# Optimization experiments

Hardware: AMD Instinct MI355X
Metric: run time of the kernel (lower is better)

Reference implementation:

```python
import jax, jax.numpy as jnp
import numpy as np

N_NODES = 50000
N_EDGES = 800000
N_GRAPHS = 2048
IN_DIM = 128
HID = 256
N_LAYERS = 4
BN_EPS = 1e-5


def setup_inputs() -> dict:
    key = jax.random.key(0)
    ks = jax.random.split(key, 12)
    x = jax.random.normal(ks[0], (N_NODES, IN_DIM), dtype=jnp.float32)
    edge_index = jax.random.randint(ks[1], (2, N_EDGES), 0, N_NODES, dtype=jnp.int64)
    batch = jnp.sort(jax.random.randint(ks[2], (N_NODES,), 0, N_GRAPHS, dtype=jnp.int64))
    convW0 = jax.random.normal(ks[3], (IN_DIM, HID), dtype=jnp.float32) * (IN_DIM ** -0.5)
    convWs = jax.random.normal(ks[4], (N_LAYERS - 1, HID, HID), dtype=jnp.float32) * (HID ** -0.5)
    convB = jnp.zeros((N_LAYERS, HID), dtype=jnp.float32)
    bn_gamma = jnp.ones((N_LAYERS, HID), dtype=jnp.float32)
    bn_beta = jnp.zeros((N_LAYERS, HID), dtype=jnp.float32)
    bn_mean = jnp.zeros((N_LAYERS, HID), dtype=jnp.float32)
    bn_var = jax.random.uniform(ks[5], (N_LAYERS, HID), dtype=jnp.float32, minval=0.5, maxval=1.5)
    lin1W = jax.random.normal(ks[6], (HID, HID // 2), dtype=jnp.float32) * (HID ** -0.5)
    lin1b = jnp.zeros((HID // 2,), dtype=jnp.float32)
    lin2W = jax.random.normal(ks[7], (HID // 2, 1), dtype=jnp.float32) * ((HID // 2) ** -0.5)
    lin2b = jnp.zeros((1,), dtype=jnp.float32)
    return dict(x=x, edge_index=edge_index, batch=batch, convW0=convW0, convWs=convWs,
                convB=convB, bn_gamma=bn_gamma, bn_beta=bn_beta, bn_mean=bn_mean,
                bn_var=bn_var, lin1W=lin1W, lin1b=lin1b, lin2W=lin2W, lin2b=lin2b)


def reference(x, edge_index, batch, convW0, convWs, convB, bn_gamma, bn_beta,
              bn_mean, bn_var, lin1W, lin1b, lin2W, lin2b):
    N = x.shape[0]
    src, dst = edge_index[0], edge_index[1]
    # degree with self-loops (PyG GCNConv default add_self_loops=True)
    deg = jnp.zeros((N,), dtype=x.dtype).at[dst].add(1.0) + 1.0
    dinv = deg ** -0.5
    enorm = (dinv[src] * dinv[dst])[:, None]      # [E,1]
    self_norm = (1.0 / deg)[:, None]              # [N,1] self-loop weight

    def gcn_conv(h, W, b):
        h = h @ W                                 # [N,H]
        agg = jax.ops.segment_sum(h[src] * enorm, dst, num_segments=N)
        return agg + h * self_norm + b

    Ws = [convW0] + [convWs[i] for i in range(convWs.shape[0])]
    for l in range(N_LAYERS):
        x = gcn_conv(x, Ws[l], convB[l])
        # eval-mode BatchNorm1d
        x = (x - bn_mean[l]) * jax.lax.rsqrt(bn_var[l] + BN_EPS) * bn_gamma[l] + bn_beta[l]
        x = jax.nn.relu(x)
        # dropout: identity in eval mode

    # global_mean_pool over graph ids
    sums = jax.ops.segment_sum(x, batch, num_segments=N_GRAPHS)      # [G,H]
    cnts = jax.ops.segment_sum(jnp.ones((N,), x.dtype), batch, num_segments=N_GRAPHS)
    pooled = sums / jnp.maximum(cnts, 1.0)[:, None]

    h = jax.nn.relu(pooled @ lin1W + lin1b)
    out = (h @ lin2W + lin2b).squeeze(-1)          # [G]
    return out
```

## Files before the change

kernel.cpp:

```cpp
#include <hip/hip_runtime.h>

#define N_NODES 50000
#define N_EDGES 800000
#define N_GRAPHS 2048
#define IN_DIM 128
#define HID 256
#define N_LAYERS 4
#define BN_EPS 1e-5f
#define NBIN 128
#define WSCALE 64.0f

#define EDGE_BLKS 3125
#define NODE_BLKS 196

typedef unsigned short ushort_t;
typedef float f32x4 __attribute__((ext_vector_type(4)));
typedef unsigned int u32x4 __attribute__((ext_vector_type(4)));
typedef _Float16 f16x8 __attribute__((ext_vector_type(8)));
typedef _Float16 f16x4 __attribute__((ext_vector_type(4)));

__device__ __forceinline__ void gl_lds16(const ushort_t* g, ushort_t* l) {
    __builtin_amdgcn_global_load_lds(
        (const __attribute__((address_space(1))) void*)g,
        (__attribute__((address_space(3))) void*)l, 16, 0, 0);
}

__global__ __launch_bounds__(256) void k_degbounds(const int* __restrict__ dst,
                                                   int* __restrict__ degi,
                                                   const int* __restrict__ batch,
                                                   int* __restrict__ gstart,
                                                   int* __restrict__ gend) {
    int bid = blockIdx.x;
    if (bid < EDGE_BLKS) {
        int e = bid * 256 + threadIdx.x;
        if (e < N_EDGES) atomicAdd(&degi[dst[e]], 1);
    } else {
        int n = (bid - EDGE_BLKS) * 256 + threadIdx.x;
        if (n >= N_NODES) return;
        int g = batch[n];
        if (n == 0 || batch[n - 1] != g) gstart[g] = n;
        if (n == N_NODES - 1 || batch[n + 1] != g) gend[g] = n + 1;
    }
}

__global__ __launch_bounds__(256) void k_nodeprep(const int* __restrict__ degi,
                                                  float* __restrict__ dinv,
                                                  float* __restrict__ selfn,
                                                  int* __restrict__ bins, int N) {
    __shared__ int lbin[NBIN];
    int t = threadIdx.x;
    if (t < NBIN) lbin[t] = 0;
    __syncthreads();
    int n = blockIdx.x * 256 + t;
    if (n < N) {
        int dg = degi[n];
        float d = 1.0f + (float)dg;
        dinv[n] = 1.0f / sqrtf(d);
        selfn[n] = 1.0f / d;
        atomicAdd(&lbin[min(dg, NBIN - 1)], 1);
    }
    __syncthreads();
    if (t < NBIN && lbin[t] > 0) atomicAdd(&bins[t], lbin[t]);
}

__global__ void k_binscan(const int* __restrict__ bins, int* __restrict__ binstart,
                          int* __restrict__ bincur, int* __restrict__ edgebase) {
    int t = threadIdx.x & 63;
    int d0 = 2 * t, d1 = 2 * t + 1;
    int a = bins[d0], b = bins[d1];
    int ea = a * d0, eb = b * d1;
    int s = a + b, es = ea + eb;
    int ps = s, pe = es;
    #pragma unroll
    for (int off = 1; off < 64; off <<= 1) {
        int u = __shfl_up(ps, off, 64);
        int v = __shfl_up(pe, off, 64);
        if (t >= off) { ps += u; pe += v; }
    }
    int exs = ps - s, exe = pe - es;
    binstart[d0] = exs;     bincur[d0] = exs;     edgebase[d0] = exe;
    binstart[d1] = exs + a; bincur[d1] = exs + a; edgebase[d1] = exe + ea;
}

__global__ __launch_bounds__(256) void k_assign(const int* __restrict__ degi,
                                                const int* __restrict__ binstart,
                                                const int* __restrict__ edgebase,
                                                const int* __restrict__ bins,
                                                int* __restrict__ bincur,
                                                int* __restrict__ perm, int* __restrict__ invperm,
                                                int2* __restrict__ meta, int* __restrict__ cursor,
                                                int N) {
    __shared__ int lbin[NBIN];
    __shared__ int lbase[NBIN];
    int t = threadIdx.x;
    if (t < NBIN) lbin[t] = 0;
    __syncthreads();
    int n = blockIdx.x * 256 + t;
    int d = 0, lrank = 0;
    if (n < N) {
        d = min(degi[n], NBIN - 1);
        lrank = atomicAdd(&lbin[d], 1);
    }
    __syncthreads();
    if (t < NBIN && lbin[t] > 0) lbase[t] = atomicAdd(&bincur[t], lbin[t]);
    __syncthreads();
    if (n < N) {
        int slot = lbase[d] + lrank;
        perm[slot] = n;
        invperm[n] = slot;
        int2 m;
        m.x = edgebase[d] + (slot - binstart[d]);
        m.y = bins[d] | (d << 20);
        meta[slot] = m;
        cursor[slot] = 0;
    }
}

__global__ __launch_bounds__(256) void k_fillprep(const int* __restrict__ src,
                                                  const int* __restrict__ dst,
                                                  const float* __restrict__ dinv,
                                                  const int* __restrict__ invperm,
                                                  const int2* __restrict__ meta,
                                                  int* __restrict__ cursor,
                                                  unsigned int* __restrict__ edata,
                                                  const float* __restrict__ gamma,
                                                  const float* __restrict__ beta,
                                                  const float* __restrict__ mean,
                                                  const float* __restrict__ var,
                                                  const float* __restrict__ bias,
                                                  const float* __restrict__ W0,
                                                  const float* __restrict__ Ws,
                                                  const float* __restrict__ x,
                                                  float* __restrict__ scale,
                                                  float* __restrict__ shift,
                                                  _Float16* __restrict__ Wh,
                                                  _Float16* __restrict__ Wl,
                                                  _Float16* __restrict__ X16) {
    int bid = blockIdx.x;
    if (bid < EDGE_BLKS) {
        int e = bid * 256 + threadIdx.x;
        if (e >= N_EDGES) return;
        int s = src[e], d = dst[e];
        int slot = invperm[d];
        int2 m = meta[slot];
        int j = atomicAdd(&cursor[slot], 1);
        int pos = m.x + j * (m.y & 0xFFFFF);
        _Float16 hw = (_Float16)(dinv[s] * dinv[d]);
        edata[pos] = ((unsigned int)__builtin_bit_cast(unsigned short, hw) << 16) |
                     (unsigned int)s;
        return;
    }
    int id = (bid - EDGE_BLKS) * 256 + threadIdx.x;
    if (id < N_LAYERS * HID) {
        float s = gamma[id] * rsqrtf(var[id] + BN_EPS);
        scale[id] = s / WSCALE;
        shift[id] = beta[id] + (bias[id] - mean[id]) * s;
        return;
    }
    id -= N_LAYERS * HID;
    const int WT = 128 * 256 + 3 * 256 * 256;
    if (id < WT) {
        float v;
        if (id < 32768) {
            int n = id >> 7, k = id & 127;
            v = W0[k * 256 + n];
        } else {
            int t = id - 32768;
            int l = t >> 16;
            int r = t & 65535;
            int n = r >> 8, k = r & 255;
            v = Ws[l * 65536 + k * 256 + n];
        }
        v *= WSCALE;
        _Float16 h = (_Float16)v;
        Wh[id] = h;
        Wl[id] = (_Float16)(v - (float)h);
        return;
    }
    id -= WT;
    const int total4 = N_NODES * IN_DIM / 4;
    if (id < total4) {
        float4 v = ((const float4*)x)[id];
        int n = id >> 5;
        int c0 = (id & 31) * 4;
        f16x4 o;
        o.x = (_Float16)v.x; o.y = (_Float16)v.y; o.z = (_Float16)v.z; o.w = (_Float16)v.w;
        *(f16x4*)(X16 + (size_t)(c0 >> 5) * (N_NODES * 32) + (size_t)n * 32 + (c0 & 31)) = o;
    }
}

__global__ __launch_bounds__(256) void k_gemm(const _Float16* __restrict__ A,
                                              const _Float16* __restrict__ Wh,
                                              const _Float16* __restrict__ Wl,
                                              const float* __restrict__ bnscale,
                                              const float* __restrict__ bnshift,
                                              _Float16* __restrict__ X16, int K) {
    __shared__ _Float16 sm[3 * 128 * 32];
    _Float16* tA  = sm;
    _Float16* tWh = sm + 4096;
    _Float16* tWl = sm + 8192;

    int tid = threadIdx.x;
    int lane = tid & 63;
    int w = tid >> 6;
    int wrow = w & 1, wcol = w >> 1;
    int row0 = blockIdx.x * 128;
    int col0 = blockIdx.y * 128;

    int srow = lane >> 2;
    int sch = lane & 3;

    f32x4 acc[4][4] = {};
    int m = lane & 15, q = lane >> 4;

    for (int k0 = 0; k0 < K; k0 += 32) {
        #pragma unroll
        for (int ii = 0; ii < 6; ++ii) {
            int G = w * 6 + ii;
            int mat = G >> 3;
            int grp = G & 7;
            const _Float16* gs = (mat == 0) ? A : (mat == 1) ? Wh : Wl;
            _Float16* ld = sm + mat * 4096;
            int rb = (mat == 0) ? row0 : col0;
            int rl = (mat == 0) ? N_NODES : (col0 + 128);
            int r = grp * 16 + srow;
            int grow = rb + r;
            int gch = sch ^ (r & 3);
            if (grow < rl)
                gl_lds16((const ushort_t*)(gs + (size_t)grow * K + k0 + gch * 8),
                         (ushort_t*)(ld + grp * 512));
        }
        __syncthreads();

        f16x8 af[4], whf[4], wlf[4];
        #pragma unroll
        for (int r = 0; r < 4; ++r) {
            int rr = wrow * 64 + r * 16 + m;
            int off = rr * 32 + ((q ^ (rr & 3)) << 3);
            af[r] = *(const f16x8*)(tA + off);
        }
        #pragma unroll
        for (int c = 0; c < 4; ++c) {
            int nn = wcol * 64 + c * 16 + m;
            int off = nn * 32 + ((q ^ (nn & 3)) << 3);
            whf[c] = *(const f16x8*)(tWh + off);
            wlf[c] = *(const f16x8*)(tWl + off);
        }
        #pragma unroll
        for (int r = 0; r < 4; ++r)
            #pragma unroll
            for (int c = 0; c < 4; ++c) {
                acc[r][c] = __builtin_amdgcn_mfma_f32_16x16x32_f16(af[r], whf[c], acc[r][c], 0, 0, 0);
                acc[r][c] = __builtin_amdgcn_mfma_f32_16x16x32_f16(af[r], wlf[c], acc[r][c], 0, 0, 0);
            }
        __syncthreads();
    }

    #pragma unroll
    for (int r = 0; r < 4; ++r) {
        int mrow = row0 + wrow * 64 + r * 16 + (lane >> 4) * 4;
        #pragma unroll
        for (int c = 0; c < 4; ++c) {
            int n = col0 + wcol * 64 + c * 16 + (lane & 15);
            float sc = bnscale[n];
            float sh = bnshift[n];
            f32x4 v = acc[r][c];
            _Float16* base = X16 + (size_t)(n >> 5) * (N_NODES * 32) + (n & 31);
            #pragma unroll
            for (int g = 0; g < 4; ++g)
                if (mrow + g < N_NODES)
                    base[(size_t)(mrow + g) * 32] =
                        (_Float16)fmaxf(fmaf(v[g], sc, sh), 0.f);
        }
    }
}

#define GNB 782

__global__ __launch_bounds__(256) void k_gather(const _Float16* __restrict__ Xc,
                                                const int2* __restrict__ meta,
                                                const unsigned int* __restrict__ edata,
                                                const int* __restrict__ perm,
                                                const float* __restrict__ selfn,
                                                _Float16* __restrict__ A,
                                                int K, int cshift) {
    int bid = blockIdx.x;
    int chunk = bid & ((1 << cshift) - 1);
    int nb = (GNB - 1) - (bid >> cshift);
    const _Float16* Hc = Xc + (size_t)chunk * (N_NODES * 32);
    int slot = nb * 64 + (threadIdx.x >> 2);
    if (slot >= N_NODES) return;
    int node = perm[slot];
    int2 m = meta[slot];
    int q8 = (threadIdx.x & 3) * 8;

    int stride = m.y & 0xFFFFF;
    int deg = m.y >> 20;
    const unsigned int* ep = edata + m.x;
    float sn = selfn[node];

    float acc[8];
    {
        f16x8 hv = *(const f16x8*)(Hc + (size_t)node * 32 + q8);
        #pragma unroll
        for (int i = 0; i < 8; ++i) acc[i] = (float)hv[i] * sn;
    }

    int j = 0;
    for (; j + 7 < deg; j += 8) {
        unsigned int e[8];
        #pragma unroll
        for (int i = 0; i < 8; ++i)
            e[i] = ep[(size_t)(j + i) * stride];
        f16x8 a[8];
        #pragma unroll
        for (int i = 0; i < 8; ++i)
            a[i] = *(const f16x8*)(Hc + (size_t)(e[i] & 0xFFFFu) * 32 + q8);
        #pragma unroll
        for (int i = 0; i < 8; ++i) {
            float w = (float)__builtin_bit_cast(_Float16, (unsigned short)(e[i] >> 16));
            #pragma unroll
            for (int c = 0; c < 8; ++c) acc[c] = fmaf((float)a[i][c], w, acc[c]);
        }
    }
    if (j + 3 < deg) {
        unsigned int e[4];
        #pragma unroll
        for (int i = 0; i < 4; ++i)
            e[i] = ep[(size_t)(j + i) * stride];
        f16x8 a[4];
        #pragma unroll
        for (int i = 0; i < 4; ++i)
            a[i] = *(const f16x8*)(Hc + (size_t)(e[i] & 0xFFFFu) * 32 + q8);
        #pragma unroll
        for (int i = 0; i < 4; ++i) {
            float w = (float)__builtin_bit_cast(_Float16, (unsigned short)(e[i] >> 16));
            #pragma unroll
            for (int c = 0; c < 8; ++c) acc[c] = fmaf((float)a[i][c], w, acc[c]);
        }
        j += 4;
    }
    for (; j < deg; ++j) {
        unsigned int e0 = ep[(size_t)j * stride];
        f16x8 a0 = *(const f16x8*)(Hc + (size_t)(e0 & 0xFFFFu) * 32 + q8);
        float w0 = (float)__builtin_bit_cast(_Float16, (unsigned short)(e0 >> 16));
        #pragma unroll
        for (int i = 0; i < 8; ++i) acc[i] = fmaf((float)a0[i], w0, acc[i]);
    }

    f16x8 o;
    #pragma unroll
    for (int i = 0; i < 8; ++i) o[i] = (_Float16)acc[i];
    u32x4 uv = *(u32x4*)&o;
    __builtin_nontemporal_store(uv, (u32x4*)(A + (size_t)node * K + chunk * 32 + q8));
}

__global__ __launch_bounds__(128) void k_poolmlp(const _Float16* __restrict__ X16,
                                                 const int* __restrict__ gstart,
                                                 const int* __restrict__ gend,
                                                 const float* __restrict__ W1,
                                                 const float* __restrict__ b1,
                                                 const float* __restrict__ W2,
                                                 const float* __restrict__ b2,
                                                 float* __restrict__ out) {
    __shared__ float prow[HID];
    __shared__ float hred[2];
    int g = blockIdx.x;
    int s = gstart[g], e = gend[g];
    int j = threadIdx.x;
    const _Float16* p0 = X16 + (size_t)(j >> 5) * (N_NODES * 32) + (j & 31);
    const _Float16* p1 = X16 + (size_t)((j >> 5) + 4) * (N_NODES * 32) + (j & 31);
    float a0 = 0.f, a1 = 0.f;
    for (int n = s; n < e; ++n) {
        a0 += (float)p0[(size_t)n * 32];
        a1 += (float)p1[(size_t)n * 32];
    }
    float inv = 1.0f / fmaxf((float)(e - s), 1.0f);
    prow[j] = a0 * inv;
    prow[j + 128] = a1 * inv;
    __syncthreads();
    float acc = 0.f;
    #pragma unroll 8
    for (int k = 0; k < HID; ++k) acc += prow[k] * W1[k * 128 + j];
    float h = fmaxf(acc + b1[j], 0.f);
    float p = h * W2[j];
    #pragma unroll
    for (int off = 32; off > 0; off >>= 1) p += __shfl_down(p, off, 64);
    if ((j & 63) == 0) hred[j >> 6] = p;
    __syncthreads();
    if (j == 0) out[g] = hred[0] + hred[1] + b2[0];
}

extern "C" void kernel_launch(void* const* d_in, const int* in_sizes, int n_in,
                              void* d_out, int out_size, void* d_ws, size_t ws_size,
                              hipStream_t stream) {
    const float* x      = (const float*)d_in[0];
    const int*   ei     = (const int*)d_in[1];
    const int*   batch  = (const int*)d_in[2];
    const float* convW0 = (const float*)d_in[3];
    const float* convWs = (const float*)d_in[4];
    const float* convB  = (const float*)d_in[5];
    const float* gamma  = (const float*)d_in[6];
    const float* beta   = (const float*)d_in[7];
    const float* mean   = (const float*)d_in[8];
    const float* var    = (const float*)d_in[9];
    const float* lin1W  = (const float*)d_in[10];
    const float* lin1b  = (const float*)d_in[11];
    const float* lin2W  = (const float*)d_in[12];
    const float* lin2b  = (const float*)d_in[13];
    float* out = (float*)d_out;

    const int* src = ei;
    const int* dst = ei + N_EDGES;

    const int WTOT = 128 * 256 + 3 * 256 * 256;

    char* wsb = (char*)d_ws;
    _Float16* x16a = (_Float16*)wsb;
    _Float16* x16b = x16a + (size_t)N_NODES * HID;
    _Float16* Ab   = x16b + (size_t)N_NODES * HID;
    _Float16* Wh16 = Ab + (size_t)N_NODES * HID;
    _Float16* Wl16 = Wh16 + WTOT;
    float* dinv    = (float*)(Wl16 + WTOT);
    float* selfn   = dinv + N_NODES;
    float* bnscale = selfn + N_NODES;
    float* bnshift = bnscale + N_LAYERS * HID;
    int*   degi    = (int*)(bnshift + N_LAYERS * HID);
    int*   bins    = degi + N_NODES;
    int*   gstart  = bins + NBIN;
    int*   gend    = gstart + N_GRAPHS;
    int*   binstart= gend + N_GRAPHS;
    int*   bincur  = binstart + NBIN;
    int*   edgebase= bincur + NBIN;
    int*   cursor  = edgebase + NBIN;
    int*   perm    = cursor + N_NODES;
    int*   invperm = perm + N_NODES;
    int2*  meta    = (int2*)(invperm + N_NODES);
    unsigned int* edata = (unsigned int*)(meta + N_NODES);

    hipMemsetAsync(degi, 0, (size_t)(N_NODES + NBIN + 2 * N_GRAPHS) * 4, stream);

    k_degbounds<<<EDGE_BLKS + NODE_BLKS, 256, 0, stream>>>(dst, degi, batch, gstart, gend);
    k_nodeprep<<<NODE_BLKS, 256, 0, stream>>>(degi, dinv, selfn, bins, N_NODES);
    k_binscan<<<1, 64, 0, stream>>>(bins, binstart, bincur, edgebase);
    k_assign<<<NODE_BLKS, 256, 0, stream>>>(degi, binstart, edgebase, bins, bincur,
                                            perm, invperm, meta, cursor, N_NODES);

    const int PREP_TOT = N_LAYERS * HID + WTOT + N_NODES * IN_DIM / 4;
    const int PREP_BLKS = (PREP_TOT + 255) / 256;
    k_fillprep<<<EDGE_BLKS + PREP_BLKS, 256, 0, stream>>>(src, dst, dinv, invperm, meta,
                                                          cursor, edata,
                                                          gamma, beta, mean, var, convB,
                                                          convW0, convWs, x,
                                                          bnscale, bnshift, Wh16, Wl16, x16a);

    dim3 gg((N_NODES + 127) / 128, 2);
    _Float16* cur = x16a;
    for (int l = 0; l < N_LAYERS; ++l) {
        int K = (l == 0) ? IN_DIM : HID;
        int nchunk = K / 32;
        int cshift = (l == 0) ? 2 : 3;
        size_t woff = (l == 0) ? 0 : (size_t)(32768 + (l - 1) * 65536);
        k_gather<<<nchunk * GNB, 256, 0, stream>>>(cur, meta, edata, perm, selfn,
                                                   Ab, K, cshift);
        _Float16* nxt = (cur == x16a) ? x16b : x16a;
        k_gemm<<<gg, 256, 0, stream>>>(Ab, Wh16 + woff, Wl16 + woff,
                                       bnscale + l * HID, bnshift + l * HID, nxt, K);
        cur = nxt;
    }

    k_poolmlp<<<N_GRAPHS, 128, 0, stream>>>(cur, gstart, gend, lin1W, lin1b, lin2W, lin2b, out);
}
```

Measured before the change: 470.9 us.

## Partition edge fill by destination slot range across XCD-interleaved blocks

The edge-fill phase now uses 8 partitions of the destination slot space. Each block reads a 2048-edge slice with vectorized nontemporal loads and handles only the edges whose destination slot falls in its partition. Block ids interleave partitions, which is likely meant to keep each partition's atomics and scattered writes local to one XCD's L2. The cost is that every edge's src/dst/invperm data is read 8 times, plus extra blocks and branch divergence.

```diff
diff --git a/kernel.cpp b/kernel.cpp
--- a/kernel.cpp
+++ b/kernel.cpp
@@ -13,9 +13,15 @@
 #define EDGE_BLKS 3125
 #define NODE_BLKS 196
 
+#define NPART 8
+#define SLOTS_PER_PART 6250
+#define FILL_SLICES 391
+#define FILL_BLKS (FILL_SLICES * NPART)
+
 typedef unsigned short ushort_t;
 typedef float f32x4 __attribute__((ext_vector_type(4)));
 typedef unsigned int u32x4 __attribute__((ext_vector_type(4)));
+typedef int i32x4 __attribute__((ext_vector_type(4)));
 typedef _Float16 f16x8 __attribute__((ext_vector_type(8)));
 typedef _Float16 f16x4 __attribute__((ext_vector_type(4)));
 
@@ -137,20 +143,54 @@
                                                   _Float16* __restrict__ Wl,
                                                   _Float16* __restrict__ X16) {
     int bid = blockIdx.x;
-    if (bid < EDGE_BLKS) {
-        int e = bid * 256 + threadIdx.x;
-        if (e >= N_EDGES) return;
-        int s = src[e], d = dst[e];
-        int slot = invperm[d];
-        int2 m = meta[slot];
-        int j = atomicAdd(&cursor[slot], 1);
-        int pos = m.x + j * (m.y & 0xFFFFF);
-        _Float16 hw = (_Float16)(dinv[s] * dinv[d]);
-        edata[pos] = ((unsigned int)__builtin_bit_cast(unsigned short, hw) << 16) |
-                     (unsigned int)s;
+    if (bid < FILL_BLKS) {
+        int part = bid & (NPART - 1);
+        int slice = bid >> 3;
+        int plo = part * SLOTS_PER_PART;
+        int phi = plo + SLOTS_PER_PART;
+        int base = slice * 2048 + threadIdx.x * 8;
+        if (base + 7 < N_EDGES) {
+            i32x4 sa = __builtin_nontemporal_load((const i32x4*)(src + base));
+            i32x4 sb = __builtin_nontemporal_load((const i32x4*)(src + base + 4));
+            i32x4 da = __builtin_nontemporal_load((const i32x4*)(dst + base));
+            i32x4 db = __builtin_nontemporal_load((const i32x4*)(dst + base + 4));
+            int s[8], d[8], slot[8];
+            #pragma unroll
+            for (int i = 0; i < 4; ++i) { s[i] = sa[i]; d[i] = da[i]; }
+            #pragma unroll
+            for (int i = 0; i < 4; ++i) { s[4 + i] = sb[i]; d[4 + i] = db[i]; }
+            #pragma unroll
+            for (int i = 0; i < 8; ++i) slot[i] = invperm[d[i]];
+            #pragma unroll
+            for (int i = 0; i < 8; ++i) {
+                if (slot[i] >= plo && slot[i] < phi) {
+                    int2 m = meta[slot[i]];
+                    int j = atomicAdd(&cursor[slot[i]], 1);
+                    int pos = m.x + j * (m.y & 0xFFFFF);
+                    _Float16 hw = (_Float16)(dinv[s[i]] * dinv[d[i]]);
+                    edata[pos] = ((unsigned int)__builtin_bit_cast(unsigned short, hw) << 16) |
+                                 (unsigned int)s[i];
+                }
+            }
+        } else {
+            for (int i = 0; i < 8; ++i) {
+                int e = base + i;
+                if (e >= N_EDGES) break;
+                int s = src[e], d = dst[e];
+                int slot = invperm[d];
+                if (slot >= plo && slot < phi) {
+                    int2 m = meta[slot];
+                    int j = atomicAdd(&cursor[slot], 1);
+                    int pos = m.x + j * (m.y & 0xFFFFF);
+                    _Float16 hw = (_Float16)(dinv[s] * dinv[d]);
+                    edata[pos] = ((unsigned int)__builtin_bit_cast(unsigned short, hw) << 16) |
+                                 (unsigned int)s;
+                }
+            }
+        }
         return;
     }
-    int id = (bid - EDGE_BLKS) * 256 + threadIdx.x;
+    int id = (bid - FILL_BLKS) * 256 + threadIdx.x;
     if (id < N_LAYERS * HID) {
         float s = gamma[id] * rsqrtf(var[id] + BN_EPS);
         scale[id] = s / WSCALE;
@@ -448,7 +488,7 @@
 
     const int PREP_TOT = N_LAYERS * HID + WTOT + N_NODES * IN_DIM / 4;
     const int PREP_BLKS = (PREP_TOT + 255) / 256;
-    k_fillprep<<<EDGE_BLKS + PREP_BLKS, 256, 0, stream>>>(src, dst, dinv, invperm, meta,
+    k_fillprep<<<FILL_BLKS + PREP_BLKS, 256, 0, stream>>>(src, dst, dinv, invperm, meta,
                                                           cursor, edata,
                                                           gamma, beta, mean, var, convB,
                                                           convW0, convWs, x,
```

Result: slower. 501.1 us (+6.4%).
